# Kernel optimization log

Measured on AMD Instinct MI355X. Metric: run time of the kernel, lower is better.

Reference implementation:

```python
import jax, jax.numpy as jnp
import numpy as np

B, N, E = 8, 4096, 65536
H, DH, GH = 4, 16, 64            # gat heads, head_dim, gat hidden
EDGE_EMBED = 16
D_FUSION = 640 + 64 + 640 + 40   # 1384


def setup_inputs() -> dict:
    key = jax.random.key(0)
    ks = jax.random.split(key, 24)
    rn = lambda i, shape, s=0.05: jax.random.normal(ks[i], shape, dtype=jnp.float32) * s
    return {
        'rnafm': rn(0, (B, 640), 1.0),
        'edit_delta': rn(1, (B, 640), 1.0),
        'hand_feat': rn(2, (B, 40), 1.0),
        'node_feats': rn(3, (B, N, 22), 1.0),
        'edge_index': jax.random.randint(ks[4], (B, 2, E), 0, N, dtype=jnp.int32),
        'edge_type': jax.random.randint(ks[5], (B, E), 0, 3, dtype=jnp.int32),
        'node_proj_w': rn(6, (GH, 22)), 'node_proj_b': jnp.zeros((GH,), jnp.float32),
        'gat_W': rn(7, (3, GH, GH)),
        'gat_a_src': rn(8, (3, H, DH)), 'gat_a_dst': rn(9, (3, H, DH)),
        'gat_a_edge': rn(10, (3, H, EDGE_EMBED)),
        'gat_edge_embed': rn(11, (3, 3, EDGE_EMBED)),
        'gat_ln_g': jnp.ones((3, GH), jnp.float32), 'gat_ln_b': jnp.zeros((3, GH), jnp.float32),
        'gat_out_w': rn(12, (64, GH)), 'gat_out_b': jnp.zeros((64,), jnp.float32),
        'enc1_w': rn(13, (256, D_FUSION)), 'enc1_b': jnp.zeros((256,), jnp.float32),
        'enc_ln_g': jnp.ones((256,), jnp.float32), 'enc_ln_b': jnp.zeros((256,), jnp.float32),
        'enc2_w': rn(14, (128, 256)), 'enc2_b': jnp.zeros((128,), jnp.float32),
        'bin_w': rn(15, (1, 128)), 'bin_b': jnp.zeros((1,), jnp.float32),
        'adp1_w': rn(16, (5, 32, 128)), 'adp1_b': jnp.zeros((5, 32), jnp.float32),
        'adp2_w': rn(17, (5, 1, 32)), 'adp2_b': jnp.zeros((5, 1), jnp.float32),
        'cls1_w': rn(18, (64, 128)), 'cls1_b': jnp.zeros((64,), jnp.float32),
        'cls2_w': rn(19, (6, 64)), 'cls2_b': jnp.zeros((6,), jnp.float32),
    }


def _layernorm(x, g, b, eps=1e-5):
    m = x.mean(-1, keepdims=True)
    v = ((x - m) ** 2).mean(-1, keepdims=True)
    return (x - m) / jnp.sqrt(v + eps) * g + b


def _gat_layer(x, src, dst, et, W, a_src, a_dst, a_edge, eemb, g, b):
    """x: [N, GH] -> [N, GH]; per-edge attention + scatter-softmax + scatter-add."""
    n = x.shape[0]
    h = x @ W.T                          # [N, GH]
    hh = h.reshape(n, H, DH)
    h_src, h_dst = hh[src], hh[dst]      # [E, H, DH] gathers
    attn = (jnp.einsum('ehd,hd->eh', h_src, a_src)
            + jnp.einsum('ehd,hd->eh', h_dst, a_dst)
            + eemb[et] @ a_edge.T)       # [E, H]
    attn = jnp.where(attn >= 0, attn, 0.2 * attn)  # leaky_relu(0.2)
    amax = jnp.maximum(jax.ops.segment_max(attn, dst, num_segments=n), -1e9)
    ex = jnp.exp(attn - amax[dst])
    denom = jax.ops.segment_sum(ex, dst, num_segments=n)
    an = ex / (denom[dst] + 1e-10)       # dropout is identity in eval
    agg = jax.ops.segment_sum(h_src * an[:, :, None], dst, num_segments=n)
    return _layernorm(agg.reshape(n, H * DH) + h, g, b)


def reference(rnafm, edit_delta, hand_feat, node_feats, edge_index, edge_type,
              node_proj_w, node_proj_b, gat_W, gat_a_src, gat_a_dst, gat_a_edge,
              gat_edge_embed, gat_ln_g, gat_ln_b, gat_out_w, gat_out_b,
              enc1_w, enc1_b, enc_ln_g, enc_ln_b, enc2_w, enc2_b,
              bin_w, bin_b, adp1_w, adp1_b, adp2_w, adp2_b,
              cls1_w, cls1_b, cls2_w, cls2_b):
    gelu = lambda t: jax.nn.gelu(t, approximate=False)

    def per_graph(nf, ei, et):
        x = nf @ node_proj_w.T + node_proj_b
        for l in range(3):
            x = gelu(_gat_layer(x, ei[0], ei[1], et, gat_W[l], gat_a_src[l],
                                gat_a_dst[l], gat_a_edge[l], gat_edge_embed[l],
                                gat_ln_g[l], gat_ln_b[l]))
        return x[x.shape[0] // 2]        # center node embedding

    gat_emb = jax.vmap(per_graph)(node_feats, edge_index, edge_type)   # [B, GH]
    gat_o = gat_emb @ gat_out_w.T + gat_out_b                          # [B, 64]
    fused = jnp.concatenate([rnafm, gat_o, edit_delta, hand_feat], axis=-1)
    h1 = _layernorm(gelu(fused @ enc1_w.T + enc1_b), enc_ln_g, enc_ln_b)
    shared = gelu(h1 @ enc2_w.T + enc2_b)                              # [B, 128]
    binary = (shared @ bin_w.T + bin_b)[:, 0]                          # [B]
    a1 = gelu(jnp.einsum('bf,hif->bhi', shared, adp1_w) + adp1_b)      # [B, 5, 32]
    per_enz = jnp.einsum('bhi,hi->bh', a1, adp2_w[:, 0, :]) + adp2_b[:, 0]  # [B, 5]
    cls = gelu(shared @ cls1_w.T + cls1_b) @ cls2_w.T + cls2_b         # [B, 6]
    return (binary, per_enz, cls, shared)
```

## Files before the change

### kernel.cpp

```cpp
#include <hip/hip_runtime.h>
#include <hip/hip_bf16.h>
#include <math.h>

#define BB 8
#define NN 4096
#define EE 65536
#define LOG2E 1.4426950408889634f

__device__ __forceinline__ float my_erf(float x){
  float ax = fabsf(x);
  float tt = 1.f/(1.f + 0.3275911f*ax);
  float poly = ((((1.061405429f*tt - 1.453152027f)*tt + 1.421413741f)*tt
                 - 0.284496736f)*tt + 0.254829592f)*tt;
  float y = 1.f - poly*expf(-ax*ax);
  return x >= 0.f ? y : -y;
}
__device__ __forceinline__ float gelu_f(float x){ return 0.5f*x*(1.0f + my_erf(x*0.7071067811865476f)); }
__device__ __forceinline__ float ld(const void* p, long i){ return ((const float*)p)[i]; }

__global__ __launch_bounds__(256) void k_pre(
    const void* __restrict__ nf, const void* __restrict__ pw, const void* __restrict__ pb,
    const void* __restrict__ W, const void* __restrict__ a_src, const void* __restrict__ a_dst,
    const void* __restrict__ a_edge, const void* __restrict__ eemb,
    const int* __restrict__ ei, const int* __restrict__ ety,
    float* __restrict__ h, float* __restrict__ sdot, float* __restrict__ ebt,
    int* __restrict__ cursor, unsigned short* __restrict__ csr,
    unsigned* __restrict__ bm1, int b0, int nb, int NF){
  int t = threadIdx.x;
  int bi = (int)blockIdx.x;
  if (NF > 0 && bi < NF){
    int bpb = NF / nb;
    int b = bi / bpb, q = bi - b*bpb;
    int e4 = q*256 + t;
    const int* base = ei + (long)(b0+b)*2*EE;
    int4 s4 = ((const int4*)base)[e4];
    int4 d4 = ((const int4*)(base + EE))[e4];
    int4 t4 = ((const int4*)(ety + (long)(b0+b)*EE))[e4];
    int* cb = cursor + b*NN;
    int ss[4] = {s4.x & (NN-1), s4.y & (NN-1), s4.z & (NN-1), s4.w & (NN-1)};
    int dd[4] = {d4.x & (NN-1), d4.y & (NN-1), d4.z & (NN-1), d4.w & (NN-1)};
    int tt[4] = {t4.x, t4.y, t4.z, t4.w};
    #pragma unroll
    for (int i=0;i<4;i++){
      int ty = tt[i]; ty = (ty < 0) ? 0 : (ty > 2 ? 2 : ty);
      int p = atomicAdd(&cb[dd[i]], 1);
      if (p < 64) csr[((long)(b*NN) + dd[i])*64 + p] = (unsigned short)(ss[i] | (ty << 12));
    }
    return;
  }
  int lb = bi - NF;

  int4 s4, d4, t4;
  bool doE = (NF == 0) && (t < 128);
  int ebb = 0;
  if (doE){
    ebb = bi & 7;
    int e4 = (bi >> 3)*128 + t;
    const int* base = ei + (long)(b0+ebb)*2*EE;
    s4 = ((const int4*)base)[e4];
    d4 = ((const int4*)(base + EE))[e4];
    t4 = ((const int4*)(ety + (long)(b0+ebb)*EE))[e4];
  }

  __attribute__((aligned(16))) __shared__ float wlT[64*68];
  __attribute__((aligned(16))) __shared__ float nfl[32*24];
  __attribute__((aligned(16))) __shared__ float xs[32*68];

  if (lb == 0 && t < 48){
    int ll = t >> 4, r = t & 15;
    if (r < 12){
      int ty = r >> 2, hd2 = r & 3;
      float s = 0.f;
      #pragma unroll
      for (int k=0;k<16;k++)
        s += ld(eemb, ll*48 + ty*16 + k) * ld(a_edge, ll*64 + hd2*16 + k);
      ebt[t] = s * LOG2E;
    }
  }
  {
    #pragma unroll
    for (int idx = t; idx < 1024; idx += 256){
      int row = idx >> 4, chunk = idx & 15;
      float4 wv = *((const float4*)((const float*)W + row*64 + chunk*4));
      *((float4*)&wlT[row*68 + chunk*4]) = wv;
    }
  }
  {
    long nfbase = ((long)b0*NN + (long)lb*32)*22;
    for (int idx = t; idx < 704; idx += 256){
      int row = idx / 22, k = idx - row*22;
      nfl[row*24 + k] = ld(nf, nfbase + idx);
    }
  }

  int w = t >> 6;
  int c = t & 63;
  int hd = c >> 4, dd2 = c & 15;
  long n0 = (long)lb*32 + w*8;

  float wreg[22];
  #pragma unroll
  for (int k = 0; k < 22; k++) wreg[k] = ld(pw, c*22 + k);
  float bias = ld(pb, c);
  __syncthreads();

  if (doE){
    int ss[4] = {s4.x & (NN-1), s4.y & (NN-1), s4.z & (NN-1), s4.w & (NN-1)};
    int dd[4] = {d4.x & (NN-1), d4.y & (NN-1), d4.z & (NN-1), d4.w & (NN-1)};
    int tt[4] = {t4.x, t4.y, t4.z, t4.w};
    #pragma unroll
    for (int i=0;i<4;i++){
      if (dd[i] == NN/2){
        int ty = tt[i]; ty = (ty < 0) ? 0 : (ty > 2 ? 2 : ty);
        int p = atomicAdd(&cursor[ebb*NN + NN/2], 1);
        if (p < 64) csr[((long)(ebb*NN) + NN/2)*64 + p] = (unsigned short)(ss[i] | (ty << 12));
        atomicOr(&bm1[ebb*128 + (ss[i] >> 5)], 1u << (ss[i] & 31));
      }
    }
  }
  if (n0 >= nb*NN) return;

  #pragma unroll
  for (int i=0;i<8;i++){
    const float* nr = nfl + (w*8+i)*24;
    float a = bias;
    #pragma unroll
    for (int kc = 0; kc < 5; kc++){
      float4 nv = *((const float4*)&nr[kc*4]);
      a += nv.x*wreg[kc*4] + nv.y*wreg[kc*4+1] + nv.z*wreg[kc*4+2] + nv.w*wreg[kc*4+3];
    }
    a += nr[20]*wreg[20] + nr[21]*wreg[21];
    xs[(w*8+i)*68 + c] = a;
  }

  float acc[8] = {0.f,0.f,0.f,0.f,0.f,0.f,0.f,0.f};
  const float* xw = xs + (w*8)*68;
  const float* wr2 = wlT + c*68;
  #pragma unroll 4
  for (int kk=0;kk<16;kk++){
    float4 wv = *((const float4*)&wr2[kk*4]);
    #pragma unroll
    for (int i=0;i<8;i++){
      float4 xv = *((const float4*)&xw[i*68 + kk*4]);
      acc[i] += xv.x*wv.x + xv.y*wv.y + xv.z*wv.z + xv.w*wv.w;
    }
  }

  float cas = ld(a_src, c) * LOG2E;
  float cad = ld(a_dst, c) * LOG2E;
  #pragma unroll
  for (int i=0;i<8;i++){
    h[(n0+i)*64 + c] = acc[i];
    float ps = acc[i]*cas, pd = acc[i]*cad;
    #pragma unroll
    for (int o=8;o>=1;o>>=1){
      ps += __shfl_xor(ps,o,64);
      pd += __shfl_xor(pd,o,64);
    }
    if (dd2 == 0){
      sdot[(n0+i)*8 + hd]     = ps;
      sdot[(n0+i)*8 + 4 + hd] = pd;
    }
  }
}

__global__ __launch_bounds__(256) void k_pass(
    const int* __restrict__ ei, const int* __restrict__ ety,
    const unsigned* __restrict__ bmA, unsigned* __restrict__ bmB,
    int* __restrict__ cursor, unsigned short* __restrict__ csr,
    int b0, int mode){
  int fi = (int)blockIdx.x;
  int b = fi & 7, q = fi >> 3;
  int e4 = q*256 + threadIdx.x;
  const int* base = ei + (long)(b0+b)*2*EE;
  int4 s4 = ((const int4*)base)[e4];
  int4 d4 = ((const int4*)(base + EE))[e4];
  int4 t4 = ((const int4*)(ety + (long)(b0+b)*EE))[e4];
  const unsigned* bA = bmA + b*128;
  unsigned* bB = bmB + b*128;
  int* cb = cursor + b*NN;
  int ss[4] = {s4.x & (NN-1), s4.y & (NN-1), s4.z & (NN-1), s4.w & (NN-1)};
  int dd[4] = {d4.x & (NN-1), d4.y & (NN-1), d4.z & (NN-1), d4.w & (NN-1)};
  int tt[4] = {t4.x, t4.y, t4.z, t4.w};
  #pragma unroll
  for (int i=0;i<4;i++){
    int d = dd[i];
    bool inA = (bA[d >> 5] >> (d & 31)) & 1u;
    bool hit;
    if (mode == 0) hit = inA && (d != NN/2);
    else {
      bool inB = (bB[d >> 5] >> (d & 31)) & 1u;
      hit = inB && !inA && (d != NN/2);
    }
    if (hit){
      int ty = tt[i]; ty = (ty < 0) ? 0 : (ty > 2 ? 2 : ty);
      int p = atomicAdd(&cb[d], 1);
      if (p < 64) csr[((long)(b*NN) + d)*64 + p] = (unsigned short)(ss[i] | (ty << 12));
      if (mode == 0) atomicOr(&bB[ss[i] >> 5], 1u << (ss[i] & 31));
    }
  }
}

__device__ __forceinline__ float gat_node(const float* __restrict__ hb,
    const float* __restrict__ sb, const unsigned short* __restrict__ cb, int dg,
    float sdP, float ebP0, float ebP1, float ebP2,
    float hdst, int c, int hd,
    const void* lng, const void* lnb, int l){
  int hL = c & 3;
  float denP = 0.f, acc = 0.f;
  int npass = (dg + 15) >> 4;
  for (int p = 0; p < npass; p++){
    int eidx = (p << 4) + (c >> 2);
    int pk = cb[eidx];
    int src = pk & 4095, ty = (pk >> 12) & 3;
    float av = sb[src*8 + hL] + sdP + (ty==0?ebP0:(ty==1?ebP1:ebP2));
    av = fmaxf(av, 0.2f*av);
    float ev = exp2f(av);
    if (eidx >= dg) ev = 0.f;
    denP += ev;
    int jmax = dg - (p << 4); if (jmax > 16) jmax = 16;
    #pragma unroll 4
    for (int j = 0; j < jmax; j++){
      float evj = __shfl(ev, j*4 + hd, 64);
      int sj = __builtin_amdgcn_readlane(pk, j*4) & 4095;
      acc += hb[(long)sj*64 + c] * evj;
    }
  }
  #pragma unroll
  for (int o=4;o<=32;o<<=1) denP += __shfl_xor(denP, o, 64);
  float den = __shfl(denP, hd, 64);
  float y = acc / (den + 1e-10f) + hdst;

  float s = y;
  #pragma unroll
  for (int o=32;o>=1;o>>=1) s += __shfl_xor(s, o, 64);
  float mean = s * (1.f/64.f);
  float d = y - mean;
  float vs = d*d;
  #pragma unroll
  for (int o=32;o>=1;o>>=1) vs += __shfl_xor(vs, o, 64);
  float var = vs * (1.f/64.f);
  float outv = d * rsqrtf(var + 1e-5f) * ld(lng, l*64+c) + ld(lnb, l*64+c);
  return gelu_f(outv);
}

__device__ __forceinline__ void gat_linear_tail(float g, float* xs, const float* wlT,
    const void* a_src, const void* a_dst, float* __restrict__ hOut,
    float* __restrict__ sdOut, long wave, int wloc, int c, int hd, int dd, int l){
  xs[wloc*68 + c] = g;
  float ha = 0.f;
  const float* xw = xs + wloc*68;
  const float* wr = wlT + c*68;
  #pragma unroll 4
  for (int kk=0;kk<16;kk++){
    float4 xv = *((const float4*)&xw[kk*4]);
    float4 wv = *((const float4*)&wr[kk*4]);
    ha += xv.x*wv.x + xv.y*wv.y + xv.z*wv.z + xv.w*wv.w;
  }
  hOut[wave*64 + c] = ha;
  float cas = ld(a_src, (long)(l+1)*64 + c) * LOG2E;
  float cad = ld(a_dst, (long)(l+1)*64 + c) * LOG2E;
  float ps = ha*cas, pd = ha*cad;
  #pragma unroll
  for (int o=8;o>=1;o>>=1){
    ps += __shfl_xor(ps,o,64);
    pd += __shfl_xor(pd,o,64);
  }
  if (dd == 0){
    sdOut[wave*8 + hd]     = ps;
    sdOut[wave*8 + 4 + hd] = pd;
  }
}

__global__ __launch_bounds__(256) void k_gatcone(
    const float* __restrict__ hIn, const float* __restrict__ sdIn,
    const float* __restrict__ ebt,
    const int* __restrict__ cursor, const unsigned short* __restrict__ csr,
    const void* __restrict__ lng, const void* __restrict__ lnb,
    const void* __restrict__ W,
    const void* __restrict__ a_src, const void* __restrict__ a_dst,
    float* __restrict__ hOut, float* __restrict__ sdOut,
    int l, int nb){
  __attribute__((aligned(16))) __shared__ float wlT[64*68];
  __attribute__((aligned(16))) __shared__ float xs[4*68];
  int t = threadIdx.x;
  int wloc = t >> 6;
  int b  = (int)blockIdx.x % nb;
  int ib = (int)blockIdx.x / nb;
  long wcen = (long)b*NN + NN/2;
  int dgc = cursor[wcen];
  dgc = (dgc < 0) ? 0 : (dgc > 64 ? 64 : dgc);
  int e0 = ib*4;
  if (e0/65 > dgc) return;
  {
    #pragma unroll
    for (int idx = t; idx < 1024; idx += 256){
      int row = idx >> 4, chunk = idx & 15;
      float4 wv = *((const float4*)((const float*)W + (long)(l+1)*4096 + row*64 + chunk*4));
      *((float4*)&wlT[row*68 + chunk*4]) = wv;
    }
  }
  __syncthreads();

  int e = e0 + wloc;
  int i = e / 65, j = e - i*65;
  long wave = -1;
  if (e < 4225 && i <= dgc){
    long vi = (i == 0) ? wcen : (long)b*NN + (csr[wcen*64 + (i-1)] & 4095);
    int dgi = cursor[vi];
    dgi = (dgi < 0) ? 0 : (dgi > 64 ? 64 : dgi);
    if (j == 0)            wave = vi;
    else if (j <= dgi)     wave = (long)b*NN + (csr[vi*64 + (j-1)] & 4095);
  }
  if (wave < 0) return;

  int c  = t & 63;
  int hd = c >> 4, dd = c & 15, hL = c & 3;

  float ebP0 = ebt[l*16 + 0 + hL];
  float ebP1 = ebt[l*16 + 4 + hL];
  float ebP2 = ebt[l*16 + 8 + hL];
  float sdP  = sdIn[wave*8 + 4 + hL];
  float hdst = hIn[wave*64 + c];
  int dg = __builtin_amdgcn_readfirstlane(cursor[wave]);
  dg = (dg < 0) ? 0 : (dg > 64 ? 64 : dg);
  const unsigned short* cb = csr + wave*64;
  const float* hb = hIn + (long)b*NN*64;
  const float* sb = sdIn + (long)b*NN*8;

  float g = gat_node(hb, sb, cb, dg, sdP, ebP0, ebP1, ebP2, hdst, c, hd, lng, lnb, l);
  gat_linear_tail(g, xs, wlT, a_src, a_dst, hOut, sdOut, wave, wloc, c, hd, dd, l);
}

__global__ __launch_bounds__(1024) void k_gat23(
    const float* __restrict__ hIn, const float* __restrict__ sdIn,
    const float* __restrict__ ebt,
    const int* __restrict__ cursor, const unsigned short* __restrict__ csr,
    const void* __restrict__ lng, const void* __restrict__ lnb,
    const void* __restrict__ W,
    const void* __restrict__ a_src, const void* __restrict__ a_dst,
    float* __restrict__ cemb, int b0, int nb){
  __attribute__((aligned(16))) __shared__ float wlT[64*68];
  __attribute__((aligned(16))) __shared__ float xsL[16*68];
  __attribute__((aligned(16))) __shared__ float h2L[65*68];
  __shared__ float sd2L[65*9];
  int t = threadIdx.x;
  int b = (int)blockIdx.x;
  if (b >= nb) return;
  {
    int row = t >> 4, chunk = t & 15;
    float4 wv = *((const float4*)((const float*)W + 2*4096 + row*64 + chunk*4));
    *((float4*)&wlT[row*68 + chunk*4]) = wv;
  }
  long wcen = (long)b*NN + NN/2;
  int dgc = cursor[wcen];
  dgc = (dgc < 0) ? 0 : (dgc > 64 ? 64 : dgc);
  int wv = t >> 6, c = t & 63;
  int hd = c >> 4, dd = c & 15, hL = c & 3;
  const float* hb = hIn + (long)b*NN*64;
  const float* sb = sdIn + (long)b*NN*8;
  float eb10 = ebt[16 + 0 + hL], eb11 = ebt[16 + 4 + hL], eb12 = ebt[16 + 8 + hL];
  float cas2 = ld(a_src, 2*64 + c) * LOG2E;
  float cad2 = ld(a_dst, 2*64 + c) * LOG2E;
  __syncthreads();

  for (int r = 0; r < 5; r++){
    int e = r*16 + wv;
    if (e < 65 && e <= dgc){
      long wave = (e == 0) ? wcen : (long)b*NN + (csr[wcen*64 + (e-1)] & 4095);
      float sdP  = sdIn[wave*8 + 4 + hL];
      float hdst = hIn[wave*64 + c];
      int dg = __builtin_amdgcn_readfirstlane(cursor[wave]);
      dg = (dg < 0) ? 0 : (dg > 64 ? 64 : dg);
      const unsigned short* cb = csr + wave*64;
      float g = gat_node(hb, sb, cb, dg, sdP, eb10, eb11, eb12, hdst, c, hd, lng, lnb, 1);
      xsL[wv*68 + c] = g;
      float ha = 0.f;
      const float* xw = xsL + wv*68;
      const float* wr = wlT + c*68;
      #pragma unroll 4
      for (int kk=0;kk<16;kk++){
        float4 xv = *((const float4*)&xw[kk*4]);
        float4 wvv = *((const float4*)&wr[kk*4]);
        ha += xv.x*wvv.x + xv.y*wvv.y + xv.z*wvv.z + xv.w*wvv.w;
      }
      h2L[e*68 + c] = ha;
      float ps = ha*cas2, pd = ha*cad2;
      #pragma unroll
      for (int o=8;o>=1;o>>=1){
        ps += __shfl_xor(ps,o,64);
        pd += __shfl_xor(pd,o,64);
      }
      if (dd == 0){
        sd2L[e*9 + hd]     = ps;
        sd2L[e*9 + 4 + hd] = pd;
      }
    }
  }
  __syncthreads();

  if (t < 64){
    float eb0 = ebt[32 + 0 + hL], eb1 = ebt[32 + 4 + hL], eb2 = ebt[32 + 8 + hL];
    float sdP  = sd2L[4 + hL];
    float hdst = h2L[c];
    int dg = dgc;
    const unsigned short* cb = csr + wcen*64;
    float denP = 0.f, acc = 0.f;
    int npass = (dg + 15) >> 4;
    for (int p = 0; p < npass; p++){
      int eidx = (p << 4) + (c >> 2);
      int pk = cb[eidx];
      int ty = (pk >> 12) & 3;
      float av = sd2L[(eidx+1)*9 + hL] + sdP + (ty==0?eb0:(ty==1?eb1:eb2));
      av = fmaxf(av, 0.2f*av);
      float ev = exp2f(av);
      if (eidx >= dg) ev = 0.f;
      denP += ev;
      int jmax = dg - (p << 4); if (jmax > 16) jmax = 16;
      #pragma unroll 4
      for (int j = 0; j < jmax; j++){
        float evj = __shfl(ev, j*4 + hd, 64);
        acc += h2L[(p*16 + j + 1)*68 + c] * evj;
      }
    }
    #pragma unroll
    for (int o=4;o<=32;o<<=1) denP += __shfl_xor(denP, o, 64);
    float den = __shfl(denP, hd, 64);
    float y = acc / (den + 1e-10f) + hdst;
    float s = y;
    #pragma unroll
    for (int o=32;o>=1;o>>=1) s += __shfl_xor(s, o, 64);
    float mean = s * (1.f/64.f);
    float d = y - mean;
    float vs = d*d;
    #pragma unroll
    for (int o=32;o>=1;o>>=1) vs += __shfl_xor(vs, o, 64);
    float var = vs * (1.f/64.f);
    float outv = d * rsqrtf(var + 1e-5f) * ld(lng, 2*64+c) + ld(lnb, 2*64+c);
    cemb[(b0+b)*64 + c] = gelu_f(outv);
  }
}

__global__ __launch_bounds__(256) void k_enc1(const float* __restrict__ ctr,
    const void* rnafm, const void* edelta, const void* hand,
    const void* gow, const void* gob,
    const void* e1w, const void* e1b, float* __restrict__ g1){
  __shared__ float fb[1384];
  __shared__ float femb[64];
  int b = blockIdx.x, t = threadIdx.x;
  for (int i=t;i<640;i+=256){
    fb[i]     = ld(rnafm,  b*640+i);
    fb[704+i] = ld(edelta, b*640+i);
  }
  if (t<40) fb[1344+t] = ld(hand, b*40+t);
  if (t>=64 && t<128){
    int cc = t-64;
    femb[cc] = ctr[b*64+cc];
  }
  __syncthreads();
  if (t<64){
    float acc = ld(gob, t);
    #pragma unroll 8
    for (int k=0;k<64;k++) acc += femb[k]*ld(gow, t*64+k);
    fb[640+t] = acc;
  }
  __syncthreads();
  int w = t >> 6, lane = t & 63;
  int c = blockIdx.y*4 + w;
  long wr = (long)c*1384;
  float acc = 0.f;
  #pragma unroll 7
  for (int i=0;i<21;i++){
    int k = lane + 64*i;
    acc += fb[k]*ld(e1w, wr+k);
  }
  if (lane < 40){
    int k = 1344+lane;
    acc += fb[k]*ld(e1w, wr+k);
  }
  #pragma unroll
  for (int o=32;o>=1;o>>=1) acc += __shfl_xor(acc, o, 64);
  if (lane==0) g1[b*256+c] = gelu_f(acc + ld(e1b, c));
}

__global__ __launch_bounds__(256) void k_enc2(const float* __restrict__ g1,
    const void* lng, const void* lnb, const void* e2w, const void* e2b,
    float* __restrict__ shs, float* __restrict__ out){
  __shared__ float red[256];
  __shared__ float h1s[256];
  int b = blockIdx.x, t = threadIdx.x;
  float g = g1[b*256+t];
  red[t] = g; __syncthreads();
  for (int s=128;s>=1;s>>=1){ if (t<s) red[t]+=red[t+s]; __syncthreads(); }
  float mean = red[0]*(1.f/256.f); __syncthreads();
  red[t] = (g-mean)*(g-mean); __syncthreads();
  for (int s=128;s>=1;s>>=1){ if (t<s) red[t]+=red[t+s]; __syncthreads(); }
  float var = red[0]*(1.f/256.f);
  h1s[t] = (g-mean)*rsqrtf(var+1e-5f)*ld(lng, t) + ld(lnb, t);
  __syncthreads();
  int w = t >> 6, lane = t & 63;
  int c = blockIdx.y*4 + w;
  long wr = (long)c*256;
  float acc = 0.f;
  #pragma unroll
  for (int i=0;i<4;i++){
    int k = lane + 64*i;
    acc += h1s[k]*ld(e2w, wr+k);
  }
  #pragma unroll
  for (int o=32;o>=1;o>>=1) acc += __shfl_xor(acc, o, 64);
  if (lane==0){
    float s = gelu_f(acc + ld(e2b, c));
    shs[b*128+c] = s;
    out[96 + b*128 + c] = s;
  }
}

__global__ __launch_bounds__(256) void k_mid(const float* __restrict__ shs,
    const void* a1w, const void* a1b, const void* c1w, const void* c1b,
    float* __restrict__ a1s, float* __restrict__ c1s){
  int b = blockIdx.x;
  int w = threadIdx.x >> 6, lane = threadIdx.x & 63;
  int idx = blockIdx.y*4 + w;
  const float* sb = shs + b*128;
  if (idx < 160){
    long wr = (long)idx*128;
    float acc = sb[lane]*ld(a1w, wr+lane) + sb[lane+64]*ld(a1w, wr+lane+64);
    #pragma unroll
    for (int o=32;o>=1;o>>=1) acc += __shfl_xor(acc, o, 64);
    if (lane==0) a1s[b*160+idx] = gelu_f(acc + ld(a1b, idx));
  } else {
    int c = idx - 160;
    long wr = (long)c*128;
    float acc = sb[lane]*ld(c1w, wr+lane) + sb[lane+64]*ld(c1w, wr+lane+64);
    #pragma unroll
    for (int o=32;o>=1;o>>=1) acc += __shfl_xor(acc, o, 64);
    if (lane==0) c1s[b*64+c] = gelu_f(acc + ld(c1b, c));
  }
}

__global__ __launch_bounds__(64) void k_fin(const float* __restrict__ shs,
    const float* __restrict__ a1s, const float* __restrict__ c1s,
    const void* binw, const void* binb, const void* a2w, const void* a2b,
    const void* c2w, const void* c2b,
    float* __restrict__ out){
  int b = blockIdx.x, t = threadIdx.x;
  {
    float p = shs[b*128+t]*ld(binw, t) + shs[b*128+t+64]*ld(binw, t+64);
    #pragma unroll
    for (int o=32;o>=1;o>>=1) p += __shfl_xor(p, o, 64);
    if (t==0) out[b] = p + ld(binb, 0);
  }
  if (t<5){
    float acc = ld(a2b, t);
    for (int i=0;i<32;i++) acc += a1s[b*160 + t*32+i]*ld(a2w, t*32+i);
    out[8 + b*5 + t] = acc;
  }
  if (t>=8 && t<14){
    int o = t-8;
    float acc = ld(c2b, o);
    for (int j=0;j<64;j++) acc += c1s[b*64+j]*ld(c2w, o*64+j);
    out[48 + b*6 + o] = acc;
  }
}

extern "C" void kernel_launch(void* const* d_in, const int* in_sizes, int n_in,
                              void* d_out, int out_size, void* d_ws, size_t ws_size,
                              hipStream_t stream) {
  const int* ei  = (const int*)d_in[4];
  const int* ety = (const int*)d_in[5];

  size_t need_full = 2048 + 512 + 16384
                   + (size_t)4*((size_t)BB*NN)
                   + (size_t)4*((size_t)BB*NN*64)
                   + (size_t)4*3*((size_t)BB*NN*64)
                   + (size_t)4*2*((size_t)BB*NN*8)
                   + (size_t)4*(8*256 + 8*128 + 8*160 + 8*64 + 64);
  int nb = (ws_size >= need_full + (1u<<20)) ? BB : 1;

  char* ws = (char*)d_ws;
  float* cemb    = (float*)ws;
  float* ebt     = (float*)(ws + 2048 + 256);
  int*   cursor  = (int*)(ws + 2048 + 512);
  int*   ticket  = cursor + (size_t)nb*NN;
  unsigned* bm1  = (unsigned*)(ticket + 64);
  unsigned* bm2  = bm1 + 8*128;
  unsigned short* csr = (unsigned short*)(bm2 + 8*128);
  float* hA      = (float*)((char*)csr + (size_t)nb*NN*64*2);
  float* hB      = hA + (size_t)nb*NN*64;
  float* sdotA   = hB + (size_t)nb*NN*64;
  float* sdotB   = sdotA + (size_t)nb*NN*8;
  float* g1      = sdotB + (size_t)nb*NN*8;
  float* shs     = g1 + 8*256;
  float* a1s     = shs + 8*128;
  float* c1s     = a1s + 8*160;

  for (int b0 = 0; b0 < BB; b0 += nb){
    hipMemsetAsync(cursor, 0, ((size_t)nb*NN + 64 + 2048)*sizeof(int), stream);
    int NL = nb*NN/32;
    int NF = (nb == BB) ? 0 : nb*(EE/1024);
    hipLaunchKernelGGL(k_pre, dim3(NF+NL), dim3(256), 0, stream,
                       d_in[3], d_in[6], d_in[7],
                       d_in[8], d_in[9], d_in[10], d_in[11], d_in[12],
                       ei, ety, hA, sdotA, ebt, cursor, csr, bm1, b0, nb, NF);
    if (nb == BB){
      hipLaunchKernelGGL(k_pass, dim3(512), dim3(256), 0, stream,
                         ei, ety, bm1, bm2, cursor, csr, b0, 0);
      hipLaunchKernelGGL(k_pass, dim3(512), dim3(256), 0, stream,
                         ei, ety, bm1, bm2, cursor, csr, b0, 1);
    }
    hipLaunchKernelGGL(k_gatcone, dim3(nb*1057), dim3(256), 0, stream,
                       hA, sdotA, ebt, cursor, csr, d_in[13], d_in[14],
                       d_in[8], d_in[9], d_in[10], hB, sdotB, 0, nb);
    hipLaunchKernelGGL(k_gat23, dim3(nb), dim3(1024), 0, stream,
                       hB, sdotB, ebt, cursor, csr, d_in[13], d_in[14],
                       d_in[8], d_in[9], d_in[10], cemb, b0, nb);
  }

  hipLaunchKernelGGL(k_enc1, dim3(BB, 64), dim3(256), 0, stream,
                     cemb,
                     d_in[0], d_in[1], d_in[2], d_in[15], d_in[16],
                     d_in[17], d_in[18], g1);
  hipLaunchKernelGGL(k_enc2, dim3(BB, 32), dim3(256), 0, stream,
                     g1, d_in[19], d_in[20], d_in[21], d_in[22], shs, (float*)d_out);
  hipLaunchKernelGGL(k_mid,  dim3(BB, 56), dim3(256), 0, stream,
                     shs, d_in[25], d_in[26], d_in[29], d_in[30], a1s, c1s);
  hipLaunchKernelGGL(k_fin,  dim3(BB), dim3(64), 0, stream,
                     shs, a1s, c1s, d_in[23], d_in[24], d_in[27], d_in[28],
                     d_in[31], d_in[32], (float*)d_out);
}
```

Baseline: 202.4 us.

## Fuse cone passes into one per-graph kernel with LDS atomics; merge tail MLP kernels

Replaces the two k_pass launches (512 blocks each, global atomics on cursor and bitmap) with one k_cone kernel per graph (8 blocks of 1024 threads). Each block keeps the cursor counters and both bitmaps in shared memory and uses LDS atomics, with a block barrier between the two passes. Separately, the enc2, mid and fin tail kernels merge into one k_tail2 kernel per batch row that holds intermediates in shared memory, and the layernorm reduction now uses wave shuffles. This removes launches and global atomic traffic, but the cone phase runs on only 8 workgroups, each scanning all edges of its graph twice serially.

Result: slower. 235.9 us (+16.5%).

```diff
diff --git a/kernel.cpp b/kernel.cpp
--- a/kernel.cpp
+++ b/kernel.cpp
@@ -164,41 +164,66 @@
   }
 }
 
-__global__ __launch_bounds__(256) void k_pass(
+__global__ __launch_bounds__(1024) void k_cone(
     const int* __restrict__ ei, const int* __restrict__ ety,
-    const unsigned* __restrict__ bmA, unsigned* __restrict__ bmB,
-    int* __restrict__ cursor, unsigned short* __restrict__ csr,
-    int b0, int mode){
-  int fi = (int)blockIdx.x;
-  int b = fi & 7, q = fi >> 3;
-  int e4 = q*256 + threadIdx.x;
+    const unsigned* __restrict__ bm1g,
+    int* __restrict__ cursor, unsigned short* __restrict__ csr, int b0){
+  __shared__ unsigned curL[NN];
+  __shared__ unsigned bm1L[128], bm2L[128];
+  int t = threadIdx.x;
+  int b = (int)blockIdx.x;
+  for (int i = t; i < NN; i += 1024) curL[i] = 0u;
+  if (t < 128){ bm1L[t] = bm1g[b*128 + t]; bm2L[t] = 0u; }
+  if (t == 0) curL[NN/2] = (unsigned)cursor[b*NN + NN/2];
+  __syncthreads();
+
   const int* base = ei + (long)(b0+b)*2*EE;
-  int4 s4 = ((const int4*)base)[e4];
-  int4 d4 = ((const int4*)(base + EE))[e4];
-  int4 t4 = ((const int4*)(ety + (long)(b0+b)*EE))[e4];
-  const unsigned* bA = bmA + b*128;
-  unsigned* bB = bmB + b*128;
-  int* cb = cursor + b*NN;
-  int ss[4] = {s4.x & (NN-1), s4.y & (NN-1), s4.z & (NN-1), s4.w & (NN-1)};
-  int dd[4] = {d4.x & (NN-1), d4.y & (NN-1), d4.z & (NN-1), d4.w & (NN-1)};
-  int tt[4] = {t4.x, t4.y, t4.z, t4.w};
-  #pragma unroll
-  for (int i=0;i<4;i++){
-    int d = dd[i];
-    bool inA = (bA[d >> 5] >> (d & 31)) & 1u;
-    bool hit;
-    if (mode == 0) hit = inA && (d != NN/2);
-    else {
-      bool inB = (bB[d >> 5] >> (d & 31)) & 1u;
-      hit = inB && !inA && (d != NN/2);
-    }
-    if (hit){
-      int ty = tt[i]; ty = (ty < 0) ? 0 : (ty > 2 ? 2 : ty);
-      int p = atomicAdd(&cb[d], 1);
-      if (p < 64) csr[((long)(b*NN) + d)*64 + p] = (unsigned short)(ss[i] | (ty << 12));
-      if (mode == 0) atomicOr(&bB[ss[i] >> 5], 1u << (ss[i] & 31));
-    }
-  }
+  const int* etyb = ety + (long)(b0+b)*EE;
+
+  for (int r = 0; r < 16; r++){
+    int e4 = r*1024 + t;
+    int4 s4 = ((const int4*)base)[e4];
+    int4 d4 = ((const int4*)(base + EE))[e4];
+    int4 t4 = ((const int4*)etyb)[e4];
+    int ss[4] = {s4.x & (NN-1), s4.y & (NN-1), s4.z & (NN-1), s4.w & (NN-1)};
+    int dd[4] = {d4.x & (NN-1), d4.y & (NN-1), d4.z & (NN-1), d4.w & (NN-1)};
+    int tt[4] = {t4.x, t4.y, t4.z, t4.w};
+    #pragma unroll
+    for (int i=0;i<4;i++){
+      int d = dd[i];
+      if (d != NN/2 && ((bm1L[d >> 5] >> (d & 31)) & 1u)){
+        int ty = tt[i]; ty = (ty < 0) ? 0 : (ty > 2 ? 2 : ty);
+        unsigned p = atomicAdd(&curL[d], 1u);
+        if (p < 64u) csr[((long)(b*NN) + d)*64 + p] = (unsigned short)(ss[i] | (ty << 12));
+        atomicOr(&bm2L[ss[i] >> 5], 1u << (ss[i] & 31));
+      }
+    }
+  }
+  __syncthreads();
+
+  for (int r = 0; r < 16; r++){
+    int e4 = r*1024 + t;
+    int4 s4 = ((const int4*)base)[e4];
+    int4 d4 = ((const int4*)(base + EE))[e4];
+    int4 t4 = ((const int4*)etyb)[e4];
+    int ss[4] = {s4.x & (NN-1), s4.y & (NN-1), s4.z & (NN-1), s4.w & (NN-1)};
+    int dd[4] = {d4.x & (NN-1), d4.y & (NN-1), d4.z & (NN-1), d4.w & (NN-1)};
+    int tt[4] = {t4.x, t4.y, t4.z, t4.w};
+    #pragma unroll
+    for (int i=0;i<4;i++){
+      int d = dd[i];
+      bool inA = (bm1L[d >> 5] >> (d & 31)) & 1u;
+      bool inB = (bm2L[d >> 5] >> (d & 31)) & 1u;
+      if (d != NN/2 && inB && !inA){
+        int ty = tt[i]; ty = (ty < 0) ? 0 : (ty > 2 ? 2 : ty);
+        unsigned p = atomicAdd(&curL[d], 1u);
+        if (p < 64u) csr[((long)(b*NN) + d)*64 + p] = (unsigned short)(ss[i] | (ty << 12));
+      }
+    }
+  }
+  __syncthreads();
+
+  for (int i = t; i < NN; i += 1024) cursor[b*NN + i] = (int)curL[i];
 }
 
 __device__ __forceinline__ float gat_node(const float* __restrict__ hb,
@@ -483,84 +508,89 @@
   if (lane==0) g1[b*256+c] = gelu_f(acc + ld(e1b, c));
 }
 
-__global__ __launch_bounds__(256) void k_enc2(const float* __restrict__ g1,
+__global__ __launch_bounds__(1024) void k_tail2(const float* __restrict__ g1,
     const void* lng, const void* lnb, const void* e2w, const void* e2b,
-    float* __restrict__ shs, float* __restrict__ out){
-  __shared__ float red[256];
+    const void* a1w, const void* a1b, const void* c1w, const void* c1b,
+    const void* binw, const void* binb, const void* a2w, const void* a2b,
+    const void* c2w, const void* c2b, float* __restrict__ out){
+  __shared__ float red[8];
   __shared__ float h1s[256];
+  __shared__ float shl[128];
+  __shared__ float a1l[160];
+  __shared__ float c1l[64];
   int b = blockIdx.x, t = threadIdx.x;
-  float g = g1[b*256+t];
-  red[t] = g; __syncthreads();
-  for (int s=128;s>=1;s>>=1){ if (t<s) red[t]+=red[t+s]; __syncthreads(); }
-  float mean = red[0]*(1.f/256.f); __syncthreads();
-  red[t] = (g-mean)*(g-mean); __syncthreads();
-  for (int s=128;s>=1;s>>=1){ if (t<s) red[t]+=red[t+s]; __syncthreads(); }
-  float var = red[0]*(1.f/256.f);
-  h1s[t] = (g-mean)*rsqrtf(var+1e-5f)*ld(lng, t) + ld(lnb, t);
-  __syncthreads();
   int w = t >> 6, lane = t & 63;
-  int c = blockIdx.y*4 + w;
-  long wr = (long)c*256;
-  float acc = 0.f;
-  #pragma unroll
-  for (int i=0;i<4;i++){
-    int k = lane + 64*i;
-    acc += h1s[k]*ld(e2w, wr+k);
-  }
-  #pragma unroll
-  for (int o=32;o>=1;o>>=1) acc += __shfl_xor(acc, o, 64);
-  if (lane==0){
-    float s = gelu_f(acc + ld(e2b, c));
-    shs[b*128+c] = s;
-    out[96 + b*128 + c] = s;
-  }
-}
-
-__global__ __launch_bounds__(256) void k_mid(const float* __restrict__ shs,
-    const void* a1w, const void* a1b, const void* c1w, const void* c1b,
-    float* __restrict__ a1s, float* __restrict__ c1s){
-  int b = blockIdx.x;
-  int w = threadIdx.x >> 6, lane = threadIdx.x & 63;
-  int idx = blockIdx.y*4 + w;
-  const float* sb = shs + b*128;
-  if (idx < 160){
-    long wr = (long)idx*128;
-    float acc = sb[lane]*ld(a1w, wr+lane) + sb[lane+64]*ld(a1w, wr+lane+64);
+
+  float g = 0.f;
+  if (t < 256) g = g1[b*256 + t];
+  float s1 = g;
+  #pragma unroll
+  for (int o=32;o>=1;o>>=1) s1 += __shfl_xor(s1, o, 64);
+  if (lane == 0 && w < 4) red[w] = s1;
+  __syncthreads();
+  float mean = (red[0]+red[1]+red[2]+red[3]) * (1.f/256.f);
+  float d = g - mean;
+  float s2 = d*d;
+  #pragma unroll
+  for (int o=32;o>=1;o>>=1) s2 += __shfl_xor(s2, o, 64);
+  if (lane == 0 && w < 4) red[4+w] = s2;
+  __syncthreads();
+  float var = (red[4]+red[5]+red[6]+red[7]) * (1.f/256.f);
+  if (t < 256) h1s[t] = d * rsqrtf(var + 1e-5f) * ld(lng, t) + ld(lnb, t);
+  __syncthreads();
+
+  #pragma unroll 2
+  for (int r = 0; r < 8; r++){
+    int c = r*16 + w;
+    long wr = (long)c*256;
+    float acc = h1s[lane]*ld(e2w, wr+lane) + h1s[lane+64]*ld(e2w, wr+lane+64)
+              + h1s[lane+128]*ld(e2w, wr+lane+128) + h1s[lane+192]*ld(e2w, wr+lane+192);
     #pragma unroll
     for (int o=32;o>=1;o>>=1) acc += __shfl_xor(acc, o, 64);
-    if (lane==0) a1s[b*160+idx] = gelu_f(acc + ld(a1b, idx));
-  } else {
-    int c = idx - 160;
-    long wr = (long)c*128;
-    float acc = sb[lane]*ld(c1w, wr+lane) + sb[lane+64]*ld(c1w, wr+lane+64);
-    #pragma unroll
-    for (int o=32;o>=1;o>>=1) acc += __shfl_xor(acc, o, 64);
-    if (lane==0) c1s[b*64+c] = gelu_f(acc + ld(c1b, c));
-  }
-}
-
-__global__ __launch_bounds__(64) void k_fin(const float* __restrict__ shs,
-    const float* __restrict__ a1s, const float* __restrict__ c1s,
-    const void* binw, const void* binb, const void* a2w, const void* a2b,
-    const void* c2w, const void* c2b,
-    float* __restrict__ out){
-  int b = blockIdx.x, t = threadIdx.x;
-  {
-    float p = shs[b*128+t]*ld(binw, t) + shs[b*128+t+64]*ld(binw, t+64);
+    if (lane == 0){
+      float sv = gelu_f(acc + ld(e2b, c));
+      shl[c] = sv;
+      out[96 + b*128 + c] = sv;
+    }
+  }
+  __syncthreads();
+
+  #pragma unroll 2
+  for (int r = 0; r < 14; r++){
+    int idx = r*16 + w;
+    if (idx < 160){
+      long wr = (long)idx*128;
+      float acc = shl[lane]*ld(a1w, wr+lane) + shl[lane+64]*ld(a1w, wr+lane+64);
+      #pragma unroll
+      for (int o=32;o>=1;o>>=1) acc += __shfl_xor(acc, o, 64);
+      if (lane==0) a1l[idx] = gelu_f(acc + ld(a1b, idx));
+    } else {
+      int c = idx - 160;
+      long wr = (long)c*128;
+      float acc = shl[lane]*ld(c1w, wr+lane) + shl[lane+64]*ld(c1w, wr+lane+64);
+      #pragma unroll
+      for (int o=32;o>=1;o>>=1) acc += __shfl_xor(acc, o, 64);
+      if (lane==0) c1l[c] = gelu_f(acc + ld(c1b, c));
+    }
+  }
+  __syncthreads();
+
+  if (w == 0){
+    float p = shl[lane]*ld(binw, lane) + shl[lane+64]*ld(binw, lane+64);
     #pragma unroll
     for (int o=32;o>=1;o>>=1) p += __shfl_xor(p, o, 64);
-    if (t==0) out[b] = p + ld(binb, 0);
-  }
-  if (t<5){
-    float acc = ld(a2b, t);
-    for (int i=0;i<32;i++) acc += a1s[b*160 + t*32+i]*ld(a2w, t*32+i);
-    out[8 + b*5 + t] = acc;
-  }
-  if (t>=8 && t<14){
-    int o = t-8;
-    float acc = ld(c2b, o);
-    for (int j=0;j<64;j++) acc += c1s[b*64+j]*ld(c2w, o*64+j);
-    out[48 + b*6 + o] = acc;
+    if (lane==0) out[b] = p + ld(binb, 0);
+    if (lane < 5){
+      float acc = ld(a2b, lane);
+      for (int i=0;i<32;i++) acc += a1l[lane*32+i]*ld(a2w, lane*32+i);
+      out[8 + b*5 + lane] = acc;
+    }
+    if (lane>=8 && lane<14){
+      int o = lane-8;
+      float acc = ld(c2b, o);
+      for (int j=0;j<64;j++) acc += c1l[j]*ld(c2w, o*64+j);
+      out[48 + b*6 + o] = acc;
+    }
   }
 }
 
@@ -604,10 +634,8 @@
                        d_in[8], d_in[9], d_in[10], d_in[11], d_in[12],
                        ei, ety, hA, sdotA, ebt, cursor, csr, bm1, b0, nb, NF);
     if (nb == BB){
-      hipLaunchKernelGGL(k_pass, dim3(512), dim3(256), 0, stream,
-                         ei, ety, bm1, bm2, cursor, csr, b0, 0);
-      hipLaunchKernelGGL(k_pass, dim3(512), dim3(256), 0, stream,
-                         ei, ety, bm1, bm2, cursor, csr, b0, 1);
+      hipLaunchKernelGGL(k_cone, dim3(8), dim3(1024), 0, stream,
+                         ei, ety, bm1, cursor, csr, b0);
     }
     hipLaunchKernelGGL(k_gatcone, dim3(nb*1057), dim3(256), 0, stream,
                        hA, sdotA, ebt, cursor, csr, d_in[13], d_in[14],
@@ -621,11 +649,10 @@
                      cemb,
                      d_in[0], d_in[1], d_in[2], d_in[15], d_in[16],
                      d_in[17], d_in[18], g1);
-  hipLaunchKernelGGL(k_enc2, dim3(BB, 32), dim3(256), 0, stream,
-                     g1, d_in[19], d_in[20], d_in[21], d_in[22], shs, (float*)d_out);
-  hipLaunchKernelGGL(k_mid,  dim3(BB, 56), dim3(256), 0, stream,
-                     shs, d_in[25], d_in[26], d_in[29], d_in[30], a1s, c1s);
-  hipLaunchKernelGGL(k_fin,  dim3(BB), dim3(64), 0, stream,
-                     shs, a1s, c1s, d_in[23], d_in[24], d_in[27], d_in[28],
+  hipLaunchKernelGGL(k_tail2, dim3(BB), dim3(1024), 0, stream,
+                     g1, d_in[19], d_in[20], d_in[21], d_in[22],
+                     d_in[25], d_in[26], d_in[29], d_in[30],
+                     d_in[23], d_in[24], d_in[27], d_in[28],
                      d_in[31], d_in[32], (float*)d_out);
-}
+  (void)shs; (void)a1s; (void)c1s;
+}
```
